# Performance work log

Hardware: AMD Instinct MI355X
Metric: run time of the kernel (lower is better)

The kernel has to match this reference:

```python
import jax, jax.numpy as jnp
import numpy as np

TEMPERATURE = 8.0  # sqrt(d_k), d_k = 64


def setup_inputs() -> dict:
    key = jax.random.key(0)
    kq, kk, kv, km = jax.random.split(key, 4)
    B, Lq, Lk, D = 64, 1024, 1024, 64
    q = jax.random.normal(kq, (B, Lq, D), dtype=jnp.float32)
    k = jax.random.normal(kk, (B, Lk, D), dtype=jnp.float32)
    v = jax.random.normal(kv, (B, Lk, D), dtype=jnp.float32)
    mask = jax.random.randint(km, (B, Lq, Lk), 0, 2).astype(jnp.bool_)
    return {"q": q, "k": k, "v": v, "mask": mask}


def reference(q, k, v, mask):
    # attn = q @ k^T / temperature, masked softmax over last dim, then @ v
    attn = jnp.einsum("bqd,bkd->bqk", q, k) / TEMPERATURE
    attn = jnp.where(mask, -jnp.inf, attn)
    attn = jax.nn.softmax(attn, axis=2)
    output = jnp.einsum("bqk,bkd->bqd", attn, v)
    return (output, attn)
```

## Files before the change

kernel.cpp:

```cpp
#include <hip/hip_runtime.h>
#include <hip/hip_bf16.h>


typedef __attribute__((ext_vector_type(8))) short bf16x8;
typedef __attribute__((ext_vector_type(4))) float f32x4;

static __device__ __forceinline__ bf16x8 pack8(float4 a, float4 b) {
    union { bf16x8 v; __hip_bfloat162 h[4]; } u;
    u.h[0] = __float22bfloat162_rn(make_float2(a.x, a.y));
    u.h[1] = __float22bfloat162_rn(make_float2(a.z, a.w));
    u.h[2] = __float22bfloat162_rn(make_float2(b.x, b.y));
    u.h[3] = __float22bfloat162_rn(make_float2(b.z, b.w));
    return u.v;
}
static __device__ __forceinline__ short f2bf(float f) {
    return (short)__builtin_bit_cast(unsigned short, __float2bfloat16(f));
}
static __device__ __forceinline__ float bf2f(short s) {
    unsigned u = ((unsigned)(unsigned short)s) << 16;
    return __builtin_bit_cast(float, u);
}

#define PIDX(r, c) ((r) * 64 + ((((c) >> 3) ^ ((r) & 7)) << 3) + ((c) & 7))

__global__ __launch_bounds__(256) void pre_maskpack(const int* __restrict__ mask,
                                                    unsigned long long* __restrict__ bits) {
    const int L = threadIdx.x & 63;
    long wid = ((long)blockIdx.x * 256 + threadIdx.x) >> 6;
    const long nwaves = (long)gridDim.x * 4;
    for (long r = wid; r < 65536; r += nwaves) {
        const int4* p = (const int4*)(mask + r * 1024 + L * 16);
        int4 a = p[0], b = p[1], c = p[2], d = p[3];
        unsigned long long bl[16];
        bl[0]  = __ballot(a.x != 0); bl[1]  = __ballot(a.y != 0);
        bl[2]  = __ballot(a.z != 0); bl[3]  = __ballot(a.w != 0);
        bl[4]  = __ballot(b.x != 0); bl[5]  = __ballot(b.y != 0);
        bl[6]  = __ballot(b.z != 0); bl[7]  = __ballot(b.w != 0);
        bl[8]  = __ballot(c.x != 0); bl[9]  = __ballot(c.y != 0);
        bl[10] = __ballot(c.z != 0); bl[11] = __ballot(c.w != 0);
        bl[12] = __ballot(d.x != 0); bl[13] = __ballot(d.y != 0);
        bl[14] = __ballot(d.z != 0); bl[15] = __ballot(d.w != 0);
        unsigned long long x = bl[0];
        #pragma unroll
        for (int j = 1; j < 16; ++j) x = (L == j) ? bl[j] : x;
        if (L < 16) bits[r * 16 + L] = x;
    }
}

__global__ __launch_bounds__(256) void pre_conv(const float* __restrict__ src,
                                                short* __restrict__ dst) {
    long i = (long)blockIdx.x * 256 + threadIdx.x;
    const float4* s = (const float4*)(src + i * 8);
    *(bf16x8*)(dst + i * 8) = pack8(s[0], s[1]);
}

__global__ __launch_bounds__(256) void pre_vtrans(const float* __restrict__ v,
                                                  short* __restrict__ vt) {
    __shared__ short t[64][72];
    const int bkt = blockIdx.x;
    const int tid = threadIdx.x;
    const int row = tid >> 2;
    const int cg  = (tid & 3) * 16;
    const float* src = v + ((long)bkt * 64 + row) * 64 + cg;
    float4 f0 = ((const float4*)src)[0];
    float4 f1 = ((const float4*)src)[1];
    float4 f2 = ((const float4*)src)[2];
    float4 f3 = ((const float4*)src)[3];
    float vv[16] = {f0.x, f0.y, f0.z, f0.w, f1.x, f1.y, f1.z, f1.w,
                    f2.x, f2.y, f2.z, f2.w, f3.x, f3.y, f3.z, f3.w};
    #pragma unroll
    for (int dd = 0; dd < 16; ++dd) t[cg + dd][row] = f2bf(vv[dd]);
    __syncthreads();
    const int d = tid >> 2, c0 = (tid & 3) * 16;
    short* dstrow = vt + (long)bkt * 4096 + d * 64;
    *(int4*)&dstrow[c0]     = *(int4*)&t[d][c0];
    *(int4*)&dstrow[c0 + 8] = *(int4*)&t[d][c0 + 8];
}

__global__ __launch_bounds__(256, 4) void attn_main(
    const float* __restrict__ q, const unsigned long long* __restrict__ bits,
    const short* __restrict__ kb, const short* __restrict__ vt,
    float* __restrict__ out, float* __restrict__ attn)
{
    __shared__ short ptile[4][16 * 64];

    const int tid  = threadIdx.x;
    const int w    = tid >> 6;
    const int L    = tid & 63;
    const int n    = L & 15;
    const int quad = L >> 4;
    const int b    = blockIdx.y;
    const long bq  = (long)b * 1024 + blockIdx.x * 64;

    const short* ktg = kb + (long)b * 65536;
    const short* vtg = vt + (long)b * 65536;

    const float* qrow = q + (bq + 16 * w + n) * 64 + quad * 8;
    float4 qa0 = ((const float4*)qrow)[0];
    float4 qa1 = ((const float4*)(qrow + 4))[0];
    float4 qb0 = ((const float4*)(qrow + 32))[0];
    float4 qb1 = ((const float4*)(qrow + 36))[0];
    const float sc = 0.125f;
    qa0.x *= sc; qa0.y *= sc; qa0.z *= sc; qa0.w *= sc;
    qa1.x *= sc; qa1.y *= sc; qa1.z *= sc; qa1.w *= sc;
    qb0.x *= sc; qb0.y *= sc; qb0.z *= sc; qb0.w *= sc;
    qb1.x *= sc; qb1.y *= sc; qb1.z *= sc; qb1.w *= sc;
    bf16x8 qf0 = pack8(qa0, qa1);
    bf16x8 qf1 = pack8(qb0, qb1);

    unsigned long long pk[4];
    #pragma unroll
    for (int i = 0; i < 4; ++i)
        pk[i] = bits[(bq + 16 * w + quad * 4 + i) * 16 + n];

    float lp[4] = {0.f, 0.f, 0.f, 0.f};
    for (int kt = 0; kt < 16; ++kt) {
        const short* kt_base = ktg + kt * 4096;
        f32x4 acc[4];
        #pragma unroll
        for (int t = 0; t < 4; ++t) { acc[t][0]=0.f; acc[t][1]=0.f; acc[t][2]=0.f; acc[t][3]=0.f; }
        #pragma unroll
        for (int t = 0; t < 4; ++t) {
            const short* krow = kt_base + (t * 16 + n) * 64 + quad * 8;
            bf16x8 b0 = *(const bf16x8*)krow;
            bf16x8 b1 = *(const bf16x8*)(krow + 32);
            acc[t] = __builtin_amdgcn_mfma_f32_16x16x32_bf16(qf0, b0, acc[t], 0, 0, 0);
            acc[t] = __builtin_amdgcn_mfma_f32_16x16x32_bf16(qf1, b1, acc[t], 0, 0, 0);
        }
        #pragma unroll
        for (int i = 0; i < 4; ++i) {
            unsigned nib = (unsigned)(pk[i] >> (4 * kt)) & 15u;
            float e0 = (nib & 1u) ? 0.f : __expf(acc[0][i]);
            float e1 = (nib & 2u) ? 0.f : __expf(acc[1][i]);
            float e2 = (nib & 4u) ? 0.f : __expf(acc[2][i]);
            float e3 = (nib & 8u) ? 0.f : __expf(acc[3][i]);
            lp[i] += (e0 + e1) + (e2 + e3);
        }
    }
    float linv[4];
    #pragma unroll
    for (int i = 0; i < 4; ++i) {
        float l = lp[i];
        l += __shfl_xor(l, 1);
        l += __shfl_xor(l, 2);
        l += __shfl_xor(l, 4);
        l += __shfl_xor(l, 8);
        linv[i] = 1.0f / l;
    }

    f32x4 oacc[4];
    #pragma unroll
    for (int t = 0; t < 4; ++t) { oacc[t][0]=0.f; oacc[t][1]=0.f; oacc[t][2]=0.f; oacc[t][3]=0.f; }

    float* attn_row = attn + (bq + 16 * w + n) * 1024;
    short* pw = ptile[w];

    for (int kt = 0; kt < 16; ++kt) {
        const short* kt_base = ktg + kt * 4096;
        f32x4 acc[4];
        #pragma unroll
        for (int t = 0; t < 4; ++t) { acc[t][0]=0.f; acc[t][1]=0.f; acc[t][2]=0.f; acc[t][3]=0.f; }
        #pragma unroll
        for (int t = 0; t < 4; ++t) {
            const short* krow = kt_base + (t * 16 + n) * 64 + quad * 8;
            bf16x8 b0 = *(const bf16x8*)krow;
            bf16x8 b1 = *(const bf16x8*)(krow + 32);
            acc[t] = __builtin_amdgcn_mfma_f32_16x16x32_bf16(qf0, b0, acc[t], 0, 0, 0);
            acc[t] = __builtin_amdgcn_mfma_f32_16x16x32_bf16(qf1, b1, acc[t], 0, 0, 0);
        }
        #pragma unroll
        for (int i = 0; i < 4; ++i) {
            unsigned nib = (unsigned)(pk[i] >> (4 * kt)) & 15u;
            float p0 = (nib & 1u) ? 0.f : __expf(acc[0][i]) * linv[i];
            float p1 = (nib & 2u) ? 0.f : __expf(acc[1][i]) * linv[i];
            float p2 = (nib & 4u) ? 0.f : __expf(acc[2][i]) * linv[i];
            float p3 = (nib & 8u) ? 0.f : __expf(acc[3][i]) * linv[i];
            int r = quad * 4 + i;
            pw[PIDX(r, n)]      = f2bf(p0);
            pw[PIDX(r, 16 + n)] = f2bf(p1);
            pw[PIDX(r, 32 + n)] = f2bf(p2);
            pw[PIDX(r, 48 + n)] = f2bf(p3);
        }
        bf16x8 pf0 = *(const bf16x8*)&pw[n * 64 + ((quad ^ (n & 7)) << 3)];
        bf16x8 pf1 = *(const bf16x8*)&pw[n * 64 + (((4 + quad) ^ (n & 7)) << 3)];
        float* ap = attn_row + kt * 64;
        float4 f0, f1, g0, g1;
        f0.x = bf2f(pf0[0]); f0.y = bf2f(pf0[1]); f0.z = bf2f(pf0[2]); f0.w = bf2f(pf0[3]);
        f1.x = bf2f(pf0[4]); f1.y = bf2f(pf0[5]); f1.z = bf2f(pf0[6]); f1.w = bf2f(pf0[7]);
        g0.x = bf2f(pf1[0]); g0.y = bf2f(pf1[1]); g0.z = bf2f(pf1[2]); g0.w = bf2f(pf1[3]);
        g1.x = bf2f(pf1[4]); g1.y = bf2f(pf1[5]); g1.z = bf2f(pf1[6]); g1.w = bf2f(pf1[7]);
        *(float4*)(ap + quad * 8)          = f0;
        *(float4*)(ap + quad * 8 + 4)      = f1;
        *(float4*)(ap + 32 + quad * 8)     = g0;
        *(float4*)(ap + 32 + quad * 8 + 4) = g1;
        const short* vt_base = vtg + kt * 4096;
        #pragma unroll
        for (int t = 0; t < 4; ++t) {
            const short* vrow = vt_base + (t * 16 + n) * 64 + quad * 8;
            bf16x8 v0 = *(const bf16x8*)vrow;
            bf16x8 v1 = *(const bf16x8*)(vrow + 32);
            oacc[t] = __builtin_amdgcn_mfma_f32_16x16x32_bf16(pf0, v0, oacc[t], 0, 0, 0);
            oacc[t] = __builtin_amdgcn_mfma_f32_16x16x32_bf16(pf1, v1, oacc[t], 0, 0, 0);
        }
    }

    #pragma unroll
    for (int t = 0; t < 4; ++t)
        #pragma unroll
        for (int i = 0; i < 4; ++i)
            out[(bq + 16 * w + quad * 4 + i) * 64 + t * 16 + n] = oacc[t][i];
}

#define KSTRIDE 72
#define PSTRIDE 68
__global__ __launch_bounds__(256) void attn_fallback(
    const float* __restrict__ q, const float* __restrict__ k,
    const float* __restrict__ v, const int* __restrict__ mask,
    float* __restrict__ out, float* __restrict__ attn)
{
    __shared__ unsigned maskbits[64][32];
    __shared__ short kbuf[64 * KSTRIDE];
    __shared__ short vtbuf[64 * KSTRIDE];
    __shared__ float ptilef[4 * 16 * PSTRIDE];

    const int tid  = threadIdx.x;
    const int w    = tid >> 6;
    const int L    = tid & 63;
    const int n    = L & 15;
    const int quad = L >> 4;
    const int b    = blockIdx.y;
    const long bq  = (long)b * 1024 + blockIdx.x * 64;

    const float* qrow = q + (bq + 16 * w + n) * 64 + quad * 8;
    float4 qa0 = ((const float4*)qrow)[0];
    float4 qa1 = ((const float4*)(qrow + 4))[0];
    float4 qb0 = ((const float4*)(qrow + 32))[0];
    float4 qb1 = ((const float4*)(qrow + 36))[0];
    const float sc = 0.125f;
    qa0.x *= sc; qa0.y *= sc; qa0.z *= sc; qa0.w *= sc;
    qa1.x *= sc; qa1.y *= sc; qa1.z *= sc; qa1.w *= sc;
    qb0.x *= sc; qb0.y *= sc; qb0.z *= sc; qb0.w *= sc;
    qb1.x *= sc; qb1.y *= sc; qb1.z *= sc; qb1.w *= sc;
    bf16x8 qf0 = pack8(qa0, qa1);
    bf16x8 qf1 = pack8(qb0, qb1);

    #pragma unroll
    for (int ii = 0; ii < 8; ++ii) {
        int wi  = ii * 256 + tid;
        int row = wi >> 5;
        int wc  = wi & 31;
        const int4* mp = (const int4*)(mask + (bq + row) * 1024 + wc * 32);
        unsigned word = 0;
        #pragma unroll
        for (int j = 0; j < 8; ++j) {
            int4 m4 = mp[j];
            word |= (m4.x != 0 ? 1u : 0u) << (4 * j + 0);
            word |= (m4.y != 0 ? 1u : 0u) << (4 * j + 1);
            word |= (m4.z != 0 ? 1u : 0u) << (4 * j + 2);
            word |= (m4.w != 0 ? 1u : 0u) << (4 * j + 3);
        }
        maskbits[row][wc] = word;
    }

    float m_i[4] = {-1e30f, -1e30f, -1e30f, -1e30f};
    float l_i[4] = {0.f, 0.f, 0.f, 0.f};

    for (int kt = 0; kt < 16; ++kt) {
        __syncthreads();
        {
            const float* kr = k + ((long)b * 1024 + kt * 64 + L) * 64 + w * 16;
            float4 k0 = ((const float4*)kr)[0];
            float4 k1 = ((const float4*)kr)[1];
            float4 k2 = ((const float4*)kr)[2];
            float4 k3 = ((const float4*)kr)[3];
            bf16x8* dst = (bf16x8*)&kbuf[L * KSTRIDE + w * 16];
            dst[0] = pack8(k0, k1);
            dst[1] = pack8(k2, k3);
        }
        __syncthreads();
        f32x4 acc[4];
        #pragma unroll
        for (int t = 0; t < 4; ++t) { acc[t][0]=0.f; acc[t][1]=0.f; acc[t][2]=0.f; acc[t][3]=0.f; }
        #pragma unroll
        for (int t = 0; t < 4; ++t) {
            bf16x8 b0 = *(const bf16x8*)&kbuf[(t * 16 + n) * KSTRIDE + quad * 8];
            bf16x8 b1 = *(const bf16x8*)&kbuf[(t * 16 + n) * KSTRIDE + 32 + quad * 8];
            acc[t] = __builtin_amdgcn_mfma_f32_16x16x32_bf16(qf0, b0, acc[t], 0, 0, 0);
            acc[t] = __builtin_amdgcn_mfma_f32_16x16x32_bf16(qf1, b1, acc[t], 0, 0, 0);
        }
        #pragma unroll
        for (int i = 0; i < 4; ++i) {
            int mrow = 16 * w + quad * 4 + i;
            unsigned w0 = maskbits[mrow][kt * 2];
            unsigned w1 = maskbits[mrow][kt * 2 + 1];
            float s0 = ((w0 >> n)        & 1u) ? -1e30f : acc[0][i];
            float s1 = ((w0 >> (16 + n)) & 1u) ? -1e30f : acc[1][i];
            float s2 = ((w1 >> n)        & 1u) ? -1e30f : acc[2][i];
            float s3 = ((w1 >> (16 + n)) & 1u) ? -1e30f : acc[3][i];
            float mt = fmaxf(fmaxf(s0, s1), fmaxf(s2, s3));
            mt = fmaxf(mt, __shfl_xor(mt, 1));
            mt = fmaxf(mt, __shfl_xor(mt, 2));
            mt = fmaxf(mt, __shfl_xor(mt, 4));
            mt = fmaxf(mt, __shfl_xor(mt, 8));
            float mnew = fmaxf(m_i[i], mt);
            float ps = __expf(s0 - mnew) + __expf(s1 - mnew)
                     + __expf(s2 - mnew) + __expf(s3 - mnew);
            ps += __shfl_xor(ps, 1);
            ps += __shfl_xor(ps, 2);
            ps += __shfl_xor(ps, 4);
            ps += __shfl_xor(ps, 8);
            l_i[i] = l_i[i] * __expf(m_i[i] - mnew) + ps;
            m_i[i] = mnew;
        }
    }
    float linv[4];
    #pragma unroll
    for (int i = 0; i < 4; ++i) linv[i] = 1.0f / l_i[i];

    f32x4 oacc[4];
    #pragma unroll
    for (int t = 0; t < 4; ++t) { oacc[t][0]=0.f; oacc[t][1]=0.f; oacc[t][2]=0.f; oacc[t][3]=0.f; }
    float* attn_row = attn + (bq + 16 * w + n) * 1024;

    for (int kt = 0; kt < 16; ++kt) {
        __syncthreads();
        {
            const float* kr = k + ((long)b * 1024 + kt * 64 + L) * 64 + w * 16;
            float4 k0 = ((const float4*)kr)[0];
            float4 k1 = ((const float4*)kr)[1];
            float4 k2 = ((const float4*)kr)[2];
            float4 k3 = ((const float4*)kr)[3];
            bf16x8* dst = (bf16x8*)&kbuf[L * KSTRIDE + w * 16];
            dst[0] = pack8(k0, k1);
            dst[1] = pack8(k2, k3);
            const float* vr = v + ((long)b * 1024 + kt * 64 + L) * 64 + w * 16;
            float4 v0 = ((const float4*)vr)[0];
            float4 v1 = ((const float4*)vr)[1];
            float4 v2 = ((const float4*)vr)[2];
            float4 v3 = ((const float4*)vr)[3];
            float vv[16] = {v0.x, v0.y, v0.z, v0.w, v1.x, v1.y, v1.z, v1.w,
                            v2.x, v2.y, v2.z, v2.w, v3.x, v3.y, v3.z, v3.w};
            #pragma unroll
            for (int dd = 0; dd < 16; ++dd)
                vtbuf[(w * 16 + dd) * KSTRIDE + L] = f2bf(vv[dd]);
        }
        __syncthreads();
        f32x4 acc[4];
        #pragma unroll
        for (int t = 0; t < 4; ++t) { acc[t][0]=0.f; acc[t][1]=0.f; acc[t][2]=0.f; acc[t][3]=0.f; }
        #pragma unroll
        for (int t = 0; t < 4; ++t) {
            bf16x8 b0 = *(const bf16x8*)&kbuf[(t * 16 + n) * KSTRIDE + quad * 8];
            bf16x8 b1 = *(const bf16x8*)&kbuf[(t * 16 + n) * KSTRIDE + 32 + quad * 8];
            acc[t] = __builtin_amdgcn_mfma_f32_16x16x32_bf16(qf0, b0, acc[t], 0, 0, 0);
            acc[t] = __builtin_amdgcn_mfma_f32_16x16x32_bf16(qf1, b1, acc[t], 0, 0, 0);
        }
        #pragma unroll
        for (int i = 0; i < 4; ++i) {
            int mrow = 16 * w + quad * 4 + i;
            unsigned w0 = maskbits[mrow][kt * 2];
            unsigned w1 = maskbits[mrow][kt * 2 + 1];
            float s0 = ((w0 >> n)        & 1u) ? -1e30f : acc[0][i];
            float s1 = ((w0 >> (16 + n)) & 1u) ? -1e30f : acc[1][i];
            float s2 = ((w1 >> n)        & 1u) ? -1e30f : acc[2][i];
            float s3 = ((w1 >> (16 + n)) & 1u) ? -1e30f : acc[3][i];
            float* pr = &ptilef[(w * 16 + quad * 4 + i) * PSTRIDE];
            pr[n]      = __expf(s0 - m_i[i]) * linv[i];
            pr[16 + n] = __expf(s1 - m_i[i]) * linv[i];
            pr[32 + n] = __expf(s2 - m_i[i]) * linv[i];
            pr[48 + n] = __expf(s3 - m_i[i]) * linv[i];
        }
        bf16x8 pf[2];
        #pragma unroll
        for (int c = 0; c < 2; ++c) {
            const float* pp = &ptilef[(w * 16 + n) * PSTRIDE + c * 32 + quad * 8];
            float4 p0 = ((const float4*)pp)[0];
            float4 p1 = ((const float4*)pp)[1];
            float* ap = attn_row + kt * 64 + c * 32 + quad * 8;
            ((float4*)ap)[0] = p0;
            ((float4*)ap)[1] = p1;
            pf[c] = pack8(p0, p1);
        }
        #pragma unroll
        for (int t = 0; t < 4; ++t) {
            bf16x8 vb0 = *(const bf16x8*)&vtbuf[(t * 16 + n) * KSTRIDE + quad * 8];
            bf16x8 vb1 = *(const bf16x8*)&vtbuf[(t * 16 + n) * KSTRIDE + 32 + quad * 8];
            oacc[t] = __builtin_amdgcn_mfma_f32_16x16x32_bf16(pf[0], vb0, oacc[t], 0, 0, 0);
            oacc[t] = __builtin_amdgcn_mfma_f32_16x16x32_bf16(pf[1], vb1, oacc[t], 0, 0, 0);
        }
    }
    #pragma unroll
    for (int t = 0; t < 4; ++t)
        #pragma unroll
        for (int i = 0; i < 4; ++i)
            out[(bq + 16 * w + quad * 4 + i) * 64 + t * 16 + n] = oacc[t][i];
}

extern "C" void kernel_launch(void* const* d_in, const int* in_sizes, int n_in,
                              void* d_out, int out_size, void* d_ws, size_t ws_size,
                              hipStream_t stream) {
    const float* q    = (const float*)d_in[0];
    const float* k    = (const float*)d_in[1];
    const float* v    = (const float*)d_in[2];
    const int*   mask = (const int*)d_in[3];
    float* out  = (float*)d_out;
    float* attn = out + (long)64 * 1024 * 64;

    dim3 grid(16, 64, 1);
    dim3 block(256, 1, 1);

    const size_t need = (size_t)24 << 20;
    if (ws_size >= need) {
        unsigned char* ws = (unsigned char*)d_ws;
        unsigned long long* bits = (unsigned long long*)ws;
        short* kbw = (short*)(ws + ((size_t)8 << 20));
        short* vtw = (short*)(ws + ((size_t)16 << 20));
        pre_maskpack<<<2048, 256, 0, stream>>>(mask, bits);
        pre_conv<<<2048, 256, 0, stream>>>(k, kbw);
        pre_vtrans<<<1024, 256, 0, stream>>>(v, vtw);
        attn_main<<<grid, block, 0, stream>>>(q, bits, kbw, vtw, out, attn);
    } else {
        attn_fallback<<<grid, block, 0, stream>>>(q, k, v, mask, out, attn);
    }
}
```

Baseline: 645.9 us.

## Stage K/V tiles into LDS via async DMA, swap MFMA operands, fuse prep kernels

The attention kernel now double-buffers swizzled bf16 K and V^T tiles in LDS using global_load_lds DMA, prefetching the next tile while computing the current one. It swaps the MFMA operand order so each lane owns one query row, which lets the fp32 attention probabilities be written directly from registers without the bf16 LDS round-trip. It also folds log2(e) into the Q scale to use exp2, simplifies mask packing to coalesced per-row ballots, and merges the K conversion and V transpose into one launch. These changes add block-wide barriers per tile and more LDS use, which may reduce occupancy.

Result: faster. 542.4 us (-16.0%).

```diff
diff --git a/kernel.cpp b/kernel.cpp
--- a/kernel.cpp
+++ b/kernel.cpp
@@ -3,8 +3,15 @@
 
 
 typedef __attribute__((ext_vector_type(8))) short bf16x8;
+typedef __attribute__((ext_vector_type(4))) short bf16x4;
 typedef __attribute__((ext_vector_type(4))) float f32x4;
 
+#define GLOBAL_AS __attribute__((address_space(1)))
+#define LDS_AS    __attribute__((address_space(3)))
+
+static __device__ __forceinline__ short f2bf(float f) {
+    return (short)__builtin_bit_cast(unsigned short, __float2bfloat16(f));
+}
 static __device__ __forceinline__ bf16x8 pack8(float4 a, float4 b) {
     union { bf16x8 v; __hip_bfloat162 h[4]; } u;
     u.h[0] = __float22bfloat162_rn(make_float2(a.x, a.y));
@@ -13,68 +20,70 @@
     u.h[3] = __float22bfloat162_rn(make_float2(b.z, b.w));
     return u.v;
 }
-static __device__ __forceinline__ short f2bf(float f) {
-    return (short)__builtin_bit_cast(unsigned short, __float2bfloat16(f));
-}
-static __device__ __forceinline__ float bf2f(short s) {
-    unsigned u = ((unsigned)(unsigned short)s) << 16;
-    return __builtin_bit_cast(float, u);
-}
-
-#define PIDX(r, c) ((r) * 64 + ((((c) >> 3) ^ ((r) & 7)) << 3) + ((c) & 7))
+static __device__ __forceinline__ bf16x4 pack4(float a, float b, float c, float d) {
+    union { bf16x4 v; __hip_bfloat162 h[2]; } u;
+    u.h[0] = __float22bfloat162_rn(make_float2(a, b));
+    u.h[1] = __float22bfloat162_rn(make_float2(c, d));
+    return u.v;
+}
+
+static __device__ __forceinline__ void dma16(void* lds, const void* g) {
+    __builtin_amdgcn_global_load_lds((const GLOBAL_AS unsigned*)g,
+                                     (LDS_AS unsigned*)lds, 16, 0, 0);
+}
+static __device__ __forceinline__ void stage8k(short* lds, const short* g, int w, int L) {
+    dma16((void*)(lds + (w * 2 + 0) * 512), (const void*)(g + (w * 2 + 0) * 512 + L * 8));
+    dma16((void*)(lds + (w * 2 + 1) * 512), (const void*)(g + (w * 2 + 1) * 512 + L * 8));
+}
 
 __global__ __launch_bounds__(256) void pre_maskpack(const int* __restrict__ mask,
                                                     unsigned long long* __restrict__ bits) {
     const int L = threadIdx.x & 63;
-    long wid = ((long)blockIdx.x * 256 + threadIdx.x) >> 6;
-    const long nwaves = (long)gridDim.x * 4;
-    for (long r = wid; r < 65536; r += nwaves) {
-        const int4* p = (const int4*)(mask + r * 1024 + L * 16);
-        int4 a = p[0], b = p[1], c = p[2], d = p[3];
-        unsigned long long bl[16];
-        bl[0]  = __ballot(a.x != 0); bl[1]  = __ballot(a.y != 0);
-        bl[2]  = __ballot(a.z != 0); bl[3]  = __ballot(a.w != 0);
-        bl[4]  = __ballot(b.x != 0); bl[5]  = __ballot(b.y != 0);
-        bl[6]  = __ballot(b.z != 0); bl[7]  = __ballot(b.w != 0);
-        bl[8]  = __ballot(c.x != 0); bl[9]  = __ballot(c.y != 0);
-        bl[10] = __ballot(c.z != 0); bl[11] = __ballot(c.w != 0);
-        bl[12] = __ballot(d.x != 0); bl[13] = __ballot(d.y != 0);
-        bl[14] = __ballot(d.z != 0); bl[15] = __ballot(d.w != 0);
-        unsigned long long x = bl[0];
-        #pragma unroll
-        for (int j = 1; j < 16; ++j) x = (L == j) ? bl[j] : x;
-        if (L < 16) bits[r * 16 + L] = x;
-    }
-}
-
-__global__ __launch_bounds__(256) void pre_conv(const float* __restrict__ src,
-                                                short* __restrict__ dst) {
-    long i = (long)blockIdx.x * 256 + threadIdx.x;
-    const float4* s = (const float4*)(src + i * 8);
-    *(bf16x8*)(dst + i * 8) = pack8(s[0], s[1]);
-}
-
-__global__ __launch_bounds__(256) void pre_vtrans(const float* __restrict__ v,
-                                                  short* __restrict__ vt) {
+    long r = ((long)blockIdx.x * 256 + threadIdx.x) >> 6;
+    const int* row = mask + r * 1024;
+    unsigned long long bl[16];
+    #pragma unroll
+    for (int kt = 0; kt < 16; ++kt)
+        bl[kt] = __ballot(row[kt * 64 + L] != 0);
+    unsigned long long x = bl[0];
+    #pragma unroll
+    for (int j = 1; j < 16; ++j) x = (L == j) ? bl[j] : x;
+    if (L < 16) bits[r * 16 + L] = x;
+}
+
+__global__ __launch_bounds__(256) void pre_kv(const float* __restrict__ k,
+                                              const float* __restrict__ v,
+                                              short* __restrict__ kb,
+                                              short* __restrict__ vt) {
     __shared__ short t[64][72];
-    const int bkt = blockIdx.x;
     const int tid = threadIdx.x;
-    const int row = tid >> 2;
-    const int cg  = (tid & 3) * 16;
-    const float* src = v + ((long)bkt * 64 + row) * 64 + cg;
-    float4 f0 = ((const float4*)src)[0];
-    float4 f1 = ((const float4*)src)[1];
-    float4 f2 = ((const float4*)src)[2];
-    float4 f3 = ((const float4*)src)[3];
-    float vv[16] = {f0.x, f0.y, f0.z, f0.w, f1.x, f1.y, f1.z, f1.w,
-                    f2.x, f2.y, f2.z, f2.w, f3.x, f3.y, f3.z, f3.w};
-    #pragma unroll
-    for (int dd = 0; dd < 16; ++dd) t[cg + dd][row] = f2bf(vv[dd]);
-    __syncthreads();
-    const int d = tid >> 2, c0 = (tid & 3) * 16;
-    short* dstrow = vt + (long)bkt * 4096 + d * 64;
-    *(int4*)&dstrow[c0]     = *(int4*)&t[d][c0];
-    *(int4*)&dstrow[c0 + 8] = *(int4*)&t[d][c0 + 8];
+    if (blockIdx.x < 2048) {
+        long ci = (long)blockIdx.x * 256 + tid;
+        long row = ci >> 3;
+        int  c   = (int)(ci & 7);
+        const float4* s = (const float4*)(k + row * 64 + c * 8);
+        int r = (int)(row & 63);
+        short* dst = kb + (row >> 6) * 4096 + (long)r * 64 + ((c ^ (r & 7)) << 3);
+        *(bf16x8*)dst = pack8(s[0], s[1]);
+    } else {
+        const int bkt = blockIdx.x - 2048;
+        const int row = tid >> 2;
+        const int cg  = (tid & 3) * 16;
+        const float* src = v + ((long)bkt * 64 + row) * 64 + cg;
+        float4 f0 = ((const float4*)src)[0];
+        float4 f1 = ((const float4*)src)[1];
+        float4 f2 = ((const float4*)src)[2];
+        float4 f3 = ((const float4*)src)[3];
+        float vv[16] = {f0.x, f0.y, f0.z, f0.w, f1.x, f1.y, f1.z, f1.w,
+                        f2.x, f2.y, f2.z, f2.w, f3.x, f3.y, f3.z, f3.w};
+        #pragma unroll
+        for (int dd = 0; dd < 16; ++dd) t[cg + dd][row] = f2bf(vv[dd]);
+        __syncthreads();
+        const int d = tid >> 2, c0 = (tid & 3) * 2;
+        short* dstrow = vt + (long)bkt * 4096 + d * 64;
+        *(int4*)&dstrow[((c0 ^ (d & 7)) << 3)]       = *(int4*)&t[d][c0 * 8];
+        *(int4*)&dstrow[(((c0 + 1) ^ (d & 7)) << 3)] = *(int4*)&t[d][c0 * 8 + 8];
+    }
 }
 
 __global__ __launch_bounds__(256, 4) void attn_main(
@@ -82,25 +91,27 @@
     const short* __restrict__ kb, const short* __restrict__ vt,
     float* __restrict__ out, float* __restrict__ attn)
 {
-    __shared__ short ptile[4][16 * 64];
+    __shared__ short kbuf[2][4096];
+    __shared__ short vbuf[2][4096];
+    __shared__ short ptile[4][1024];
 
     const int tid  = threadIdx.x;
     const int w    = tid >> 6;
     const int L    = tid & 63;
     const int n    = L & 15;
-    const int quad = L >> 4;
+    const int g    = L >> 4;
     const int b    = blockIdx.y;
     const long bq  = (long)b * 1024 + blockIdx.x * 64;
 
     const short* ktg = kb + (long)b * 65536;
     const short* vtg = vt + (long)b * 65536;
 
-    const float* qrow = q + (bq + 16 * w + n) * 64 + quad * 8;
+    const float* qrow = q + (bq + 16 * w + n) * 64 + g * 8;
     float4 qa0 = ((const float4*)qrow)[0];
     float4 qa1 = ((const float4*)(qrow + 4))[0];
     float4 qb0 = ((const float4*)(qrow + 32))[0];
     float4 qb1 = ((const float4*)(qrow + 36))[0];
-    const float sc = 0.125f;
+    const float sc = 0.125f * 1.4426950408889634f;
     qa0.x *= sc; qa0.y *= sc; qa0.z *= sc; qa0.w *= sc;
     qa1.x *= sc; qa1.y *= sc; qa1.z *= sc; qa1.w *= sc;
     qb0.x *= sc; qb0.y *= sc; qb0.z *= sc; qb0.w *= sc;
@@ -108,107 +119,103 @@
     bf16x8 qf0 = pack8(qa0, qa1);
     bf16x8 qf1 = pack8(qb0, qb1);
 
-    unsigned long long pk[4];
-    #pragma unroll
-    for (int i = 0; i < 4; ++i)
-        pk[i] = bits[(bq + 16 * w + quad * 4 + i) * 16 + n];
-
-    float lp[4] = {0.f, 0.f, 0.f, 0.f};
+    const unsigned long long* mrow_ptr = bits + (bq + 16 * w + n) * 16;
+    const int sw = (n & 7);
+
+    float lp = 0.f;
+    stage8k(kbuf[0], ktg, w, L);
+    __syncthreads();
+
     for (int kt = 0; kt < 16; ++kt) {
-        const short* kt_base = ktg + kt * 4096;
+        if (kt < 15) {
+            stage8k(kbuf[(kt + 1) & 1], ktg + (kt + 1) * 4096, w, L);
+        } else {
+            stage8k(kbuf[0], ktg, w, L);
+            stage8k(vbuf[0], vtg, w, L);
+        }
+        unsigned long long mrow = mrow_ptr[kt];
+        const short* kl = kbuf[kt & 1];
         f32x4 acc[4];
         #pragma unroll
         for (int t = 0; t < 4; ++t) { acc[t][0]=0.f; acc[t][1]=0.f; acc[t][2]=0.f; acc[t][3]=0.f; }
         #pragma unroll
         for (int t = 0; t < 4; ++t) {
-            const short* krow = kt_base + (t * 16 + n) * 64 + quad * 8;
-            bf16x8 b0 = *(const bf16x8*)krow;
-            bf16x8 b1 = *(const bf16x8*)(krow + 32);
-            acc[t] = __builtin_amdgcn_mfma_f32_16x16x32_bf16(qf0, b0, acc[t], 0, 0, 0);
-            acc[t] = __builtin_amdgcn_mfma_f32_16x16x32_bf16(qf1, b1, acc[t], 0, 0, 0);
-        }
-        #pragma unroll
-        for (int i = 0; i < 4; ++i) {
-            unsigned nib = (unsigned)(pk[i] >> (4 * kt)) & 15u;
-            float e0 = (nib & 1u) ? 0.f : __expf(acc[0][i]);
-            float e1 = (nib & 2u) ? 0.f : __expf(acc[1][i]);
-            float e2 = (nib & 4u) ? 0.f : __expf(acc[2][i]);
-            float e3 = (nib & 8u) ? 0.f : __expf(acc[3][i]);
-            lp[i] += (e0 + e1) + (e2 + e3);
-        }
-    }
-    float linv[4];
-    #pragma unroll
-    for (int i = 0; i < 4; ++i) {
-        float l = lp[i];
-        l += __shfl_xor(l, 1);
-        l += __shfl_xor(l, 2);
-        l += __shfl_xor(l, 4);
-        l += __shfl_xor(l, 8);
-        linv[i] = 1.0f / l;
-    }
+            bf16x8 kf0 = *(const bf16x8*)&kl[(t * 16 + n) * 64 + ((g ^ sw) << 3)];
+            bf16x8 kf1 = *(const bf16x8*)&kl[(t * 16 + n) * 64 + (((4 + g) ^ sw) << 3)];
+            acc[t] = __builtin_amdgcn_mfma_f32_16x16x32_bf16(kf0, qf0, acc[t], 0, 0, 0);
+            acc[t] = __builtin_amdgcn_mfma_f32_16x16x32_bf16(kf1, qf1, acc[t], 0, 0, 0);
+        }
+        unsigned long long ms = mrow >> (g * 4);
+        #pragma unroll
+        for (int t = 0; t < 4; ++t)
+            #pragma unroll
+            for (int i = 0; i < 4; ++i) {
+                unsigned bit = (unsigned)(ms >> (t * 16 + i)) & 1u;
+                lp += bit ? 0.f : __builtin_exp2f(acc[t][i]);
+            }
+        __syncthreads();
+    }
+    float l = lp + __shfl_xor(lp, 16);
+    l += __shfl_xor(l, 32);
+    const float linv = 1.0f / l;
 
     f32x4 oacc[4];
     #pragma unroll
-    for (int t = 0; t < 4; ++t) { oacc[t][0]=0.f; oacc[t][1]=0.f; oacc[t][2]=0.f; oacc[t][3]=0.f; }
+    for (int u = 0; u < 4; ++u) { oacc[u][0]=0.f; oacc[u][1]=0.f; oacc[u][2]=0.f; oacc[u][3]=0.f; }
 
     float* attn_row = attn + (bq + 16 * w + n) * 1024;
     short* pw = ptile[w];
 
     for (int kt = 0; kt < 16; ++kt) {
-        const short* kt_base = ktg + kt * 4096;
+        if (kt < 15) {
+            stage8k(kbuf[(kt + 1) & 1], ktg + (kt + 1) * 4096, w, L);
+            stage8k(vbuf[(kt + 1) & 1], vtg + (kt + 1) * 4096, w, L);
+        }
+        unsigned long long mrow = mrow_ptr[kt];
+        const short* kl = kbuf[kt & 1];
+        const short* vl = vbuf[kt & 1];
         f32x4 acc[4];
         #pragma unroll
         for (int t = 0; t < 4; ++t) { acc[t][0]=0.f; acc[t][1]=0.f; acc[t][2]=0.f; acc[t][3]=0.f; }
         #pragma unroll
         for (int t = 0; t < 4; ++t) {
-            const short* krow = kt_base + (t * 16 + n) * 64 + quad * 8;
-            bf16x8 b0 = *(const bf16x8*)krow;
-            bf16x8 b1 = *(const bf16x8*)(krow + 32);
-            acc[t] = __builtin_amdgcn_mfma_f32_16x16x32_bf16(qf0, b0, acc[t], 0, 0, 0);
-            acc[t] = __builtin_amdgcn_mfma_f32_16x16x32_bf16(qf1, b1, acc[t], 0, 0, 0);
-        }
-        #pragma unroll
-        for (int i = 0; i < 4; ++i) {
-            unsigned nib = (unsigned)(pk[i] >> (4 * kt)) & 15u;
-            float p0 = (nib & 1u) ? 0.f : __expf(acc[0][i]) * linv[i];
-            float p1 = (nib & 2u) ? 0.f : __expf(acc[1][i]) * linv[i];
-            float p2 = (nib & 4u) ? 0.f : __expf(acc[2][i]) * linv[i];
-            float p3 = (nib & 8u) ? 0.f : __expf(acc[3][i]) * linv[i];
-            int r = quad * 4 + i;
-            pw[PIDX(r, n)]      = f2bf(p0);
-            pw[PIDX(r, 16 + n)] = f2bf(p1);
-            pw[PIDX(r, 32 + n)] = f2bf(p2);
-            pw[PIDX(r, 48 + n)] = f2bf(p3);
-        }
-        bf16x8 pf0 = *(const bf16x8*)&pw[n * 64 + ((quad ^ (n & 7)) << 3)];
-        bf16x8 pf1 = *(const bf16x8*)&pw[n * 64 + (((4 + quad) ^ (n & 7)) << 3)];
-        float* ap = attn_row + kt * 64;
-        float4 f0, f1, g0, g1;
-        f0.x = bf2f(pf0[0]); f0.y = bf2f(pf0[1]); f0.z = bf2f(pf0[2]); f0.w = bf2f(pf0[3]);
-        f1.x = bf2f(pf0[4]); f1.y = bf2f(pf0[5]); f1.z = bf2f(pf0[6]); f1.w = bf2f(pf0[7]);
-        g0.x = bf2f(pf1[0]); g0.y = bf2f(pf1[1]); g0.z = bf2f(pf1[2]); g0.w = bf2f(pf1[3]);
-        g1.x = bf2f(pf1[4]); g1.y = bf2f(pf1[5]); g1.z = bf2f(pf1[6]); g1.w = bf2f(pf1[7]);
-        *(float4*)(ap + quad * 8)          = f0;
-        *(float4*)(ap + quad * 8 + 4)      = f1;
-        *(float4*)(ap + 32 + quad * 8)     = g0;
-        *(float4*)(ap + 32 + quad * 8 + 4) = g1;
-        const short* vt_base = vtg + kt * 4096;
-        #pragma unroll
-        for (int t = 0; t < 4; ++t) {
-            const short* vrow = vt_base + (t * 16 + n) * 64 + quad * 8;
-            bf16x8 v0 = *(const bf16x8*)vrow;
-            bf16x8 v1 = *(const bf16x8*)(vrow + 32);
-            oacc[t] = __builtin_amdgcn_mfma_f32_16x16x32_bf16(pf0, v0, oacc[t], 0, 0, 0);
-            oacc[t] = __builtin_amdgcn_mfma_f32_16x16x32_bf16(pf1, v1, oacc[t], 0, 0, 0);
-        }
-    }
-
-    #pragma unroll
-    for (int t = 0; t < 4; ++t)
+            bf16x8 kf0 = *(const bf16x8*)&kl[(t * 16 + n) * 64 + ((g ^ sw) << 3)];
+            bf16x8 kf1 = *(const bf16x8*)&kl[(t * 16 + n) * 64 + (((4 + g) ^ sw) << 3)];
+            acc[t] = __builtin_amdgcn_mfma_f32_16x16x32_bf16(kf0, qf0, acc[t], 0, 0, 0);
+            acc[t] = __builtin_amdgcn_mfma_f32_16x16x32_bf16(kf1, qf1, acc[t], 0, 0, 0);
+        }
+        unsigned long long ms = mrow >> (g * 4);
+        #pragma unroll
+        for (int t = 0; t < 4; ++t) {
+            unsigned b0 = (unsigned)(ms >> (t * 16 + 0)) & 1u;
+            unsigned b1 = (unsigned)(ms >> (t * 16 + 1)) & 1u;
+            unsigned b2 = (unsigned)(ms >> (t * 16 + 2)) & 1u;
+            unsigned b3 = (unsigned)(ms >> (t * 16 + 3)) & 1u;
+            float p0 = b0 ? 0.f : __builtin_exp2f(acc[t][0]) * linv;
+            float p1 = b1 ? 0.f : __builtin_exp2f(acc[t][1]) * linv;
+            float p2 = b2 ? 0.f : __builtin_exp2f(acc[t][2]) * linv;
+            float p3 = b3 ? 0.f : __builtin_exp2f(acc[t][3]) * linv;
+            *(float4*)(attn_row + kt * 64 + t * 16 + g * 4) = make_float4(p0, p1, p2, p3);
+            *(bf16x4*)&pw[n * 64 + ((((t * 2) + (g >> 1)) ^ sw) << 3) + (g & 1) * 4] =
+                pack4(p0, p1, p2, p3);
+        }
+        bf16x8 pf0 = *(const bf16x8*)&pw[n * 64 + ((g ^ sw) << 3)];
+        bf16x8 pf1 = *(const bf16x8*)&pw[n * 64 + (((4 + g) ^ sw) << 3)];
+        #pragma unroll
+        for (int u = 0; u < 4; ++u) {
+            bf16x8 vf0 = *(const bf16x8*)&vl[(u * 16 + n) * 64 + ((g ^ sw) << 3)];
+            bf16x8 vf1 = *(const bf16x8*)&vl[(u * 16 + n) * 64 + (((4 + g) ^ sw) << 3)];
+            oacc[u] = __builtin_amdgcn_mfma_f32_16x16x32_bf16(pf0, vf0, oacc[u], 0, 0, 0);
+            oacc[u] = __builtin_amdgcn_mfma_f32_16x16x32_bf16(pf1, vf1, oacc[u], 0, 0, 0);
+        }
+        __syncthreads();
+    }
+
+    #pragma unroll
+    for (int u = 0; u < 4; ++u)
         #pragma unroll
         for (int i = 0; i < 4; ++i)
-            out[(bq + 16 * w + quad * 4 + i) * 64 + t * 16 + n] = oacc[t][i];
+            out[(bq + 16 * w + g * 4 + i) * 64 + u * 16 + n] = oacc[u][i];
 }
 
 #define KSTRIDE 72
@@ -415,9 +422,8 @@
         unsigned long long* bits = (unsigned long long*)ws;
         short* kbw = (short*)(ws + ((size_t)8 << 20));
         short* vtw = (short*)(ws + ((size_t)16 << 20));
-        pre_maskpack<<<2048, 256, 0, stream>>>(mask, bits);
-        pre_conv<<<2048, 256, 0, stream>>>(k, kbw);
-        pre_vtrans<<<1024, 256, 0, stream>>>(v, vtw);
+        pre_maskpack<<<16384, 256, 0, stream>>>(mask, bits);
+        pre_kv<<<3072, 256, 0, stream>>>(k, v, kbw, vtw);
         attn_main<<<grid, block, 0, stream>>>(q, bits, kbw, vtw, out, attn);
     } else {
         attn_fallback<<<grid, block, 0, stream>>>(q, k, v, mask, out, attn);
```
